# Kernel optimization log

Hardware: AMD Instinct MI355X
Metric: run time of the kernel (lower is better)

Reference implementation:

```python
import jax, jax.numpy as jnp
import numpy as np

N, E, G = 100000, 600000, 2000
CONV = [128, 256, 256, 256]
LIN = [256, 128, 1]
BN_EPS = 1e-5


def setup_inputs() -> dict:
    key = jax.random.key(0)
    ks = iter(jax.random.split(key, 64))
    inp = {}
    inp["x"] = jax.random.normal(next(ks), (N, CONV[0]), dtype=jnp.float32)
    inp["edge_index"] = jax.random.randint(next(ks), (2, E), 0, N)
    inp["batch"] = jnp.sort(jax.random.randint(next(ks), (N,), 0, G))

    def lin_w(k, i, o):
        return (jax.random.normal(k, (i, o), dtype=jnp.float32) / np.sqrt(i)).astype(jnp.float32)

    # 3 GINConv MLPs: Linear(in,out), BN(out), ReLU, Linear(out,out), ReLU
    for i in range(3):
        ci, co = CONV[i], CONV[i + 1]
        inp[f"c{i}_w1"] = lin_w(next(ks), ci, co)
        inp[f"c{i}_b1"] = jnp.zeros((co,), jnp.float32)
        inp[f"c{i}_g"] = jnp.ones((co,), jnp.float32)
        inp[f"c{i}_be"] = jnp.zeros((co,), jnp.float32)
        inp[f"c{i}_m"] = jax.random.normal(next(ks), (co,), dtype=jnp.float32) * 0.1
        inp[f"c{i}_v"] = jax.random.uniform(next(ks), (co,), minval=0.5, maxval=1.5, dtype=jnp.float32)
        inp[f"c{i}_w2"] = lin_w(next(ks), co, co)
        inp[f"c{i}_b2"] = jnp.zeros((co,), jnp.float32)
    # head: Linear(256,128) + BN(128) + ReLU, Linear(128,1)
    inp["l0_w"] = lin_w(next(ks), LIN[0], LIN[1])
    inp["l0_b"] = jnp.zeros((LIN[1],), jnp.float32)
    inp["l0_g"] = jnp.ones((LIN[1],), jnp.float32)
    inp["l0_be"] = jnp.zeros((LIN[1],), jnp.float32)
    inp["l0_m"] = jax.random.normal(next(ks), (LIN[1],), dtype=jnp.float32) * 0.1
    inp["l0_v"] = jax.random.uniform(next(ks), (LIN[1],), minval=0.5, maxval=1.5, dtype=jnp.float32)
    inp["l1_w"] = lin_w(next(ks), LIN[1], LIN[2])
    inp["l1_b"] = jnp.zeros((LIN[2],), jnp.float32)
    return inp


def _bn(h, g, be, m, v):
    return g * (h - m) * jax.lax.rsqrt(v + BN_EPS) + be


def _gin_conv(x, src, dst, w1, b1, g, be, m, v, w2, b2):
    # GINConv (eps=0): MLP(x + sum_{j in N(i)} x_j); messages x[src] aggregated at dst
    agg = jax.ops.segment_sum(x[src], dst, num_segments=x.shape[0])
    h = (x + agg) @ w1 + b1
    h = jax.nn.relu(_bn(h, g, be, m, v))
    return jax.nn.relu(h @ w2 + b2)


def reference(x, edge_index, batch,
              c0_w1, c0_b1, c0_g, c0_be, c0_m, c0_v, c0_w2, c0_b2,
              c1_w1, c1_b1, c1_g, c1_be, c1_m, c1_v, c1_w2, c1_b2,
              c2_w1, c2_b1, c2_g, c2_be, c2_m, c2_v, c2_w2, c2_b2,
              l0_w, l0_b, l0_g, l0_be, l0_m, l0_v, l1_w, l1_b):
    src, dst = edge_index[0], edge_index[1]
    conv_params = [
        (c0_w1, c0_b1, c0_g, c0_be, c0_m, c0_v, c0_w2, c0_b2),
        (c1_w1, c1_b1, c1_g, c1_be, c1_m, c1_v, c1_w2, c1_b2),
        (c2_w1, c2_b1, c2_g, c2_be, c2_m, c2_v, c2_w2, c2_b2),
    ]
    h = x
    for i, p in enumerate(conv_params):
        h = _gin_conv(h, src, dst, *p)
        if i < 2:
            h = jax.nn.relu(h)  # outer activation (no-op after ReLU, kept for fidelity)
    # global_add_pool over graphs
    h = jax.ops.segment_sum(h, batch, num_segments=G)  # [G, 256]
    h = h @ l0_w + l0_b
    h = _bn(h, l0_g, l0_be, l0_m, l0_v)
    h = jax.nn.relu(h)  # dropout is identity in eval mode
    return h @ l1_w + l1_b  # [G, 1]
```

## Files before the change

kernel.cpp:

```cpp
#include <hip/hip_runtime.h>
#include <hip/hip_bf16.h>

#define BN_EPS 1e-5f

typedef __attribute__((ext_vector_type(8))) short short8;
typedef __attribute__((ext_vector_type(4))) float f32x4;

__device__ __forceinline__ void gll16(const void* g, void* l) {
    __builtin_amdgcn_global_load_lds(
        (const __attribute__((address_space(1))) unsigned int*)g,
        (__attribute__((address_space(3))) unsigned int*)l, 16, 0, 0);
}

__device__ __forceinline__ unsigned pack_bf2(float a, float b) {
    __hip_bfloat16 ba = __float2bfloat16(a);
    __hip_bfloat16 bb = __float2bfloat16(b);
    return (unsigned)(*(unsigned short*)&ba) | ((unsigned)(*(unsigned short*)&bb) << 16);
}

__global__ void hist_kernel(const int* __restrict__ dst, int* __restrict__ off, int E) {
    int e = blockIdx.x * blockDim.x + threadIdx.x;
    if (e < E) atomicAdd(&off[dst[e] + 1], 1);
}

__global__ __launch_bounds__(256) void scan1_kernel(int* __restrict__ data,
                                                    int* __restrict__ sums, int n) {
    __shared__ int sh[256];
    const int t = threadIdx.x;
    const int idx = blockIdx.x * 1024 + t * 4;
    int v[4];
    int s = 0;
#pragma unroll
    for (int j = 0; j < 4; ++j) {
        int x = (idx + j < n) ? data[idx + j] : 0;
        s += x;
        v[j] = s;
    }
    sh[t] = s;
    __syncthreads();
    for (int o = 1; o < 256; o <<= 1) {
        int x = (t >= o) ? sh[t - o] : 0;
        __syncthreads();
        sh[t] += x;
        __syncthreads();
    }
    const int prev = sh[t] - s;
#pragma unroll
    for (int j = 0; j < 4; ++j) {
        if (idx + j < n) data[idx + j] = v[j] + prev;
    }
    if (t == 255) sums[blockIdx.x] = sh[255];
}

__global__ __launch_bounds__(256) void scan2_kernel(int* __restrict__ sums, int nb) {
    __shared__ int sh[256];
    const int t = threadIdx.x;
    sh[t] = (t < nb) ? sums[t] : 0;
    __syncthreads();
    for (int o = 1; o < 256; o <<= 1) {
        int x = (t >= o) ? sh[t - o] : 0;
        __syncthreads();
        sh[t] += x;
        __syncthreads();
    }
    if (t < nb) sums[t] = sh[t];
}

__global__ void scan3_kernel(int* __restrict__ data, const int* __restrict__ sums,
                             int* __restrict__ cursor, int n, int N) {
    int i = blockIdx.x * blockDim.x + threadIdx.x;
    if (i >= n) return;
    int b = i >> 10;
    int v = data[i];
    if (b > 0) { v += sums[b - 1]; data[i] = v; }
    if (i < N) cursor[i] = v;
}

__global__ void fill_kernel(const int* __restrict__ src, const int* __restrict__ dst,
                            int* __restrict__ cursor, int* __restrict__ sorted_src, int E) {
    int e = blockIdx.x * blockDim.x + threadIdx.x;
    if (e >= E) return;
    int p = atomicAdd(&cursor[dst[e]], 1);
    sorted_src[p] = src[e];
}

__global__ void cvt_x_kernel(const float* __restrict__ x, __hip_bfloat16* __restrict__ xb,
                             int N, int total4 ) {
    int i = blockIdx.x * blockDim.x + threadIdx.x;
    if (i >= total4) return;
    int n = i >> 5;
    unsigned lo = 0, hi = 0;
    if (n < N) {
        const float4 v = ((const float4*)x)[i];
        lo = pack_bf2(v.x, v.y);
        hi = pack_bf2(v.z, v.w);
    }
    ((uint2*)xb)[i] = make_uint2(lo, hi);
}

__global__ void wt_all_kernel(const float* __restrict__ w0, const float* __restrict__ w1,
                              const float* __restrict__ w2, const float* __restrict__ w3,
                              const float* __restrict__ w4, const float* __restrict__ w5,
                              __hip_bfloat16* __restrict__ o0, __hip_bfloat16* __restrict__ o1,
                              __hip_bfloat16* __restrict__ o2, __hip_bfloat16* __restrict__ o3,
                              __hip_bfloat16* __restrict__ o4, __hip_bfloat16* __restrict__ o5) {
    int i = blockIdx.x * blockDim.x + threadIdx.x;
    const int S0 = 256 * 128, S = 256 * 256;
    if (i < S0) {
        int m = i / 128, k = i - m * 128;
        o0[i] = __float2bfloat16(w0[k * 256 + m]);
        return;
    }
    i -= S0;
    int mi = i / S, j = i - mi * S;
    if (mi >= 5) return;
    int m = j >> 8, k = j & 255;
    const float* Wp; __hip_bfloat16* Op;
    switch (mi) {
        case 0: Wp = w1; Op = o1; break;
        case 1: Wp = w2; Op = o2; break;
        case 2: Wp = w3; Op = o3; break;
        case 3: Wp = w4; Op = o4; break;
        default: Wp = w5; Op = o5; break;
    }
    Op[j] = __float2bfloat16(Wp[k * 256 + m]);
}

__global__ void prep_ss_kernel(
    const float* __restrict__ g0, const float* __restrict__ be0, const float* __restrict__ m0,
    const float* __restrict__ v0, const float* __restrict__ b10, const float* __restrict__ b20,
    const float* __restrict__ g1, const float* __restrict__ be1, const float* __restrict__ m1,
    const float* __restrict__ v1, const float* __restrict__ b11, const float* __restrict__ b21,
    const float* __restrict__ g2, const float* __restrict__ be2, const float* __restrict__ m2,
    const float* __restrict__ v2, const float* __restrict__ b12, const float* __restrict__ b22,
    float* __restrict__ ss) {
    const int layer = blockIdx.x;
    const int c = threadIdx.x;
    const float *g, *be, *m, *v, *b1, *b2;
    switch (layer) {
        case 0: g = g0; be = be0; m = m0; v = v0; b1 = b10; b2 = b20; break;
        case 1: g = g1; be = be1; m = m1; v = v1; b1 = b11; b2 = b21; break;
        default: g = g2; be = be2; m = m2; v = v2; b1 = b12; b2 = b22; break;
    }
    float r = rsqrtf(v[c] + BN_EPS);
    float s = g[c] * r;
    ss[(2 * layer) * 512 + c] = s;
    ss[(2 * layer) * 512 + 256 + c] = (b1[c] - m[c]) * s + be[c];
    ss[(2 * layer + 1) * 512 + c] = 1.f;
    ss[(2 * layer + 1) * 512 + 256 + c] = b2[c];
}

template <int C>
__global__ __launch_bounds__(256) void agg_fused(const __hip_bfloat16* __restrict__ h,
                                                 const int* __restrict__ off,
                                                 const int* __restrict__ ssrc,
                                                 __hip_bfloat16* __restrict__ out, int N) {
    constexpr int L = C / 8;
    int t = blockIdx.x * blockDim.x + threadIdx.x;
    int n = t / L;
    if (n >= N) return;
    int c8 = t - n * L;
    const uint4* hp = (const uint4*)h;

    float acc[8];
    {
        uint4 sv = hp[(size_t)n * L + c8];
        const unsigned u[4] = {sv.x, sv.y, sv.z, sv.w};
#pragma unroll
        for (int j = 0; j < 4; ++j) {
            acc[2 * j]     = __uint_as_float(u[j] << 16);
            acc[2 * j + 1] = __uint_as_float(u[j] & 0xffff0000u);
        }
    }
    const int e0 = off[n], e1 = off[n + 1];
    int e = e0;
    for (; e + 2 <= e1; e += 2) {
        int s0 = ssrc[e], s1 = ssrc[e + 1];
        uint4 a = hp[(size_t)s0 * L + c8];
        uint4 b = hp[(size_t)s1 * L + c8];
        const unsigned ua[4] = {a.x, a.y, a.z, a.w};
        const unsigned ub[4] = {b.x, b.y, b.z, b.w};
#pragma unroll
        for (int j = 0; j < 4; ++j) {
            acc[2 * j]     += __uint_as_float(ua[j] << 16);
            acc[2 * j + 1] += __uint_as_float(ua[j] & 0xffff0000u);
            acc[2 * j]     += __uint_as_float(ub[j] << 16);
            acc[2 * j + 1] += __uint_as_float(ub[j] & 0xffff0000u);
        }
    }
    if (e < e1) {
        int s0 = ssrc[e];
        uint4 a = hp[(size_t)s0 * L + c8];
        const unsigned ua[4] = {a.x, a.y, a.z, a.w};
#pragma unroll
        for (int j = 0; j < 4; ++j) {
            acc[2 * j]     += __uint_as_float(ua[j] << 16);
            acc[2 * j + 1] += __uint_as_float(ua[j] & 0xffff0000u);
        }
    }
    unsigned o[4];
#pragma unroll
    for (int j = 0; j < 4; ++j) o[j] = pack_bf2(acc[2 * j], acc[2 * j + 1]);
    ((uint4*)out)[(size_t)n * L + c8] = make_uint4(o[0], o[1], o[2], o[3]);
}

template <int K1>
__global__ __launch_bounds__(512, 4) void mlp_fused(
    const __hip_bfloat16* __restrict__ A,
    const __hip_bfloat16* __restrict__ W1t,
    const __hip_bfloat16* __restrict__ W2t,
    const float* __restrict__ ss1, const float* __restrict__ ss2,
    __hip_bfloat16* __restrict__ C) {
    __shared__ __align__(16) char bufT[32 * 1024];

    const int tid = threadIdx.x;
    const int l   = tid & 63;
    const int w   = tid >> 6;
    const size_t row0 = (size_t)blockIdx.x * 64;

    constexpr int ROWB = K1 * 2;
    constexpr int NT1  = K1 / 32;
    const int l15  = l & 15;
    const int kg   = l >> 4;
    const int lswz = (l & 7) << 4;

    {
        const char* Ab = (const char*)(A + row0 * K1);
        constexpr int NIA = 64 * ROWB / 1024;
        constexpr int RPI = 1024 / ROWB;
#pragma unroll
        for (int i = w; i < NIA; i += 8) {
            int row = i * RPI + (l * 16) / ROWB;
            int byt = ((l * 16) % ROWB) ^ ((row & 7) << 4);
            gll16(Ab + (size_t)row * ROWB + byt, bufT + i * 1024);
        }
    }
    asm volatile("s_waitcnt vmcnt(0)" ::: "memory");
    __syncthreads();

    f32x4 acc1[2][4] = {};
    {
        const char* wp0 = (const char*)W1t + (size_t)(w * 32 + l15) * ROWB + kg * 16;
        const char* wp1 = wp0 + 16 * ROWB;
#pragma unroll
        for (int t = 0; t < NT1; ++t) {
            const short8 wf0 = *(const short8*)(wp0 + t * 64);
            const short8 wf1 = *(const short8*)(wp1 + t * 64);
            short8 af[4];
            const int abyt = (t * 64 + kg * 16) ^ lswz;
#pragma unroll
            for (int j = 0; j < 4; ++j)
                af[j] = *(const short8*)(bufT + (j * 16 + l15) * ROWB + abyt);
#pragma unroll
            for (int j = 0; j < 4; ++j) {
                acc1[0][j] = __builtin_amdgcn_mfma_f32_16x16x32_bf16(wf0, af[j], acc1[0][j], 0, 0, 0);
                acc1[1][j] = __builtin_amdgcn_mfma_f32_16x16x32_bf16(wf1, af[j], acc1[1][j], 0, 0, 0);
            }
        }
    }
    __syncthreads();

#pragma unroll
    for (int i = 0; i < 2; ++i) {
        const int m0 = w * 32 + i * 16 + kg * 4;
        const float4 s4 = *(const float4*)(ss1 + m0);
        const float4 h4 = *(const float4*)(ss1 + 256 + m0);
        const int byt = (m0 * 2) ^ lswz;
#pragma unroll
        for (int j = 0; j < 4; ++j) {
            const int n = j * 16 + l15;
            const float v0 = fmaxf(acc1[i][j][0] * s4.x + h4.x, 0.f);
            const float v1 = fmaxf(acc1[i][j][1] * s4.y + h4.y, 0.f);
            const float v2 = fmaxf(acc1[i][j][2] * s4.z + h4.z, 0.f);
            const float v3 = fmaxf(acc1[i][j][3] * s4.w + h4.w, 0.f);
            *(uint2*)(bufT + n * 512 + byt) = make_uint2(pack_bf2(v0, v1), pack_bf2(v2, v3));
        }
    }
    __syncthreads();

    f32x4 acc2[2][4] = {};
    {
        const char* wp0 = (const char*)W2t + (size_t)(w * 32 + l15) * 512 + kg * 16;
        const char* wp1 = wp0 + 16 * 512;
#pragma unroll
        for (int t = 0; t < 8; ++t) {
            const short8 wf0 = *(const short8*)(wp0 + t * 64);
            const short8 wf1 = *(const short8*)(wp1 + t * 64);
            short8 tf[4];
            const int tbyt = (t * 64 + kg * 16) ^ lswz;
#pragma unroll
            for (int j = 0; j < 4; ++j)
                tf[j] = *(const short8*)(bufT + (j * 16 + l15) * 512 + tbyt);
#pragma unroll
            for (int j = 0; j < 4; ++j) {
                acc2[0][j] = __builtin_amdgcn_mfma_f32_16x16x32_bf16(wf0, tf[j], acc2[0][j], 0, 0, 0);
                acc2[1][j] = __builtin_amdgcn_mfma_f32_16x16x32_bf16(wf1, tf[j], acc2[1][j], 0, 0, 0);
            }
        }
    }
    __syncthreads();

#pragma unroll
    for (int i = 0; i < 2; ++i) {
        const int c0 = w * 32 + i * 16 + kg * 4;
        const float4 s4 = *(const float4*)(ss2 + c0);
        const float4 h4 = *(const float4*)(ss2 + 256 + c0);
        const int byt = (c0 * 2) ^ lswz;
#pragma unroll
        for (int j = 0; j < 4; ++j) {
            const int n = j * 16 + l15;
            const float v0 = fmaxf(acc2[i][j][0] * s4.x + h4.x, 0.f);
            const float v1 = fmaxf(acc2[i][j][1] * s4.y + h4.y, 0.f);
            const float v2 = fmaxf(acc2[i][j][2] * s4.z + h4.z, 0.f);
            const float v3 = fmaxf(acc2[i][j][3] * s4.w + h4.w, 0.f);
            *(uint2*)(bufT + n * 512 + byt) = make_uint2(pack_bf2(v0, v1), pack_bf2(v2, v3));
        }
    }
    __syncthreads();

    {
        char* Cb = (char*)C + row0 * 512;
#pragma unroll
        for (int q = tid; q < 2048; q += 512) {
            const int n = q >> 5;
            const int slot = (q & 31) * 16;
            uint4 v = *(const uint4*)(bufT + n * 512 + (slot ^ ((n & 7) << 4)));
            *(uint4*)(Cb + q * 16) = v;
        }
    }
}

__device__ __forceinline__ int lower_bound_dev(const int* __restrict__ a, int n, int key) {
    int lo = 0, hi = n;
    while (lo < hi) {
        int mid = (lo + hi) >> 1;
        if (a[mid] < key) lo = mid + 1; else hi = mid;
    }
    return lo;
}

__global__ __launch_bounds__(256) void pool_seg_kernel(const __hip_bfloat16* __restrict__ h,
                                                       const int* __restrict__ batch,
                                                       float* __restrict__ pooled, int N) {
    __shared__ int seg[2];
    const int g = blockIdx.x;
    if (threadIdx.x == 0) seg[0] = lower_bound_dev(batch, N, g);
    if (threadIdx.x == 1) seg[1] = lower_bound_dev(batch, N, g + 1);
    __syncthreads();
    const int c = threadIdx.x;
    float acc = 0.f;
    for (int n = seg[0]; n < seg[1]; ++n) acc += __bfloat162float(h[(size_t)n * 256 + c]);
    pooled[(size_t)g * 256 + c] = acc;
}

__global__ __launch_bounds__(128) void head_kernel(
    const float* __restrict__ pooled,
    const float* __restrict__ w0, const float* __restrict__ b0,
    const float* __restrict__ g, const float* __restrict__ be,
    const float* __restrict__ m, const float* __restrict__ v,
    const float* __restrict__ w1, const float* __restrict__ b1,
    float* __restrict__ out) {
    __shared__ float row[256];
    __shared__ float red[128];
    const int gid = blockIdx.x;
    const int j = threadIdx.x;

    row[j]       = pooled[(size_t)gid * 256 + j];
    row[j + 128] = pooled[(size_t)gid * 256 + 128 + j];
    __syncthreads();

    float acc = b0[j];
#pragma unroll 8
    for (int k = 0; k < 256; ++k) acc += row[k] * w0[k * 128 + j];

    float h = g[j] * (acc - m[j]) * rsqrtf(v[j] + BN_EPS) + be[j];
    h = fmaxf(h, 0.f) * w1[j];
    red[j] = h;
    __syncthreads();
    for (int s = 64; s > 0; s >>= 1) {
        if (j < s) red[j] += red[j + s];
        __syncthreads();
    }
    if (j == 0) out[gid] = red[0] + b1[0];
}

extern "C" void kernel_launch(void* const* d_in, const int* in_sizes, int n_in,
                              void* d_out, int out_size, void* d_ws, size_t ws_size,
                              hipStream_t stream) {
    const float* x    = (const float*)d_in[0];
    const int* eidx   = (const int*)d_in[1];
    const int* batch  = (const int*)d_in[2];

    const int N = in_sizes[0] / 128;
    const int E = in_sizes[1] / 2;
    const int G = out_size;

    const int* src = eidx;
    const int* dst = eidx + E;

    const float* cw1[3]; const float* cb1[3]; const float* cg[3]; const float* cbe[3];
    const float* cm[3];  const float* cv[3];  const float* cw2[3]; const float* cb2[3];
    for (int i = 0; i < 3; ++i) {
        int b = 3 + i * 8;
        cw1[i] = (const float*)d_in[b + 0];
        cb1[i] = (const float*)d_in[b + 1];
        cg[i]  = (const float*)d_in[b + 2];
        cbe[i] = (const float*)d_in[b + 3];
        cm[i]  = (const float*)d_in[b + 4];
        cv[i]  = (const float*)d_in[b + 5];
        cw2[i] = (const float*)d_in[b + 6];
        cb2[i] = (const float*)d_in[b + 7];
    }
    const float* l0_w  = (const float*)d_in[27];
    const float* l0_b  = (const float*)d_in[28];
    const float* l0_g  = (const float*)d_in[29];
    const float* l0_be = (const float*)d_in[30];
    const float* l0_m  = (const float*)d_in[31];
    const float* l0_v  = (const float*)d_in[32];
    const float* l1_w  = (const float*)d_in[33];
    const float* l1_b  = (const float*)d_in[34];

    float* outp = (float*)d_out;

    const int nrb  = (N + 127) / 128;
    const int Npad = nrb * 128;
    const int nrb64 = Npad / 64;
    const size_t SB = (size_t)Npad * 256 * 2;
    const size_t XB = (size_t)Npad * 128 * 2;
    const size_t PB = (size_t)G * 256 * 4;
    const size_t WTB = (size_t)256 * 256 * 2;

    char* ws = (char*)d_ws;
    size_t o = 0;
    __hip_bfloat16* U  = (__hip_bfloat16*)(ws + o); o += SB;
    __hip_bfloat16* V  = (__hip_bfloat16*)(ws + o); o += SB;
    __hip_bfloat16* xb = (__hip_bfloat16*)(ws + o); o += XB;
    float* pooled      = (float*)(ws + o);       o += PB;
    __hip_bfloat16* wt[6];
    for (int i = 0; i < 6; ++i) { wt[i] = (__hip_bfloat16*)(ws + o); o += WTB; }
    float* ss          = (float*)(ws + o);       o += 6 * 512 * 4;
    int* csr_off    = (int*)(ws + o); o += (size_t)(N + 1) * 4;
    int* cursor     = (int*)(ws + o); o += (size_t)N * 4;
    int* sorted_src = (int*)(ws + o); o += (size_t)E * 4;
    int* sums       = (int*)(ws + o); o += 256 * 4;
    if (ws_size < o) return;

    const dim3 blk(256);

    {
        int total4 = Npad * 128 / 4;
        cvt_x_kernel<<<(total4 + 255) / 256, blk, 0, stream>>>(x, xb, N, total4);
    }
    {
        int total = 256 * 128 + 5 * 256 * 256;
        wt_all_kernel<<<(total + 255) / 256, blk, 0, stream>>>(
            cw1[0], cw2[0], cw1[1], cw2[1], cw1[2], cw2[2],
            wt[0], wt[1], wt[2], wt[3], wt[4], wt[5]);
    }
    prep_ss_kernel<<<3, blk, 0, stream>>>(
        cg[0], cbe[0], cm[0], cv[0], cb1[0], cb2[0],
        cg[1], cbe[1], cm[1], cv[1], cb1[1], cb2[1],
        cg[2], cbe[2], cm[2], cv[2], cb1[2], cb2[2], ss);

    {
        const int n_off = N + 1;
        hipMemsetAsync(csr_off, 0, (size_t)n_off * sizeof(int), stream);
        hist_kernel<<<(E + 255) / 256, blk, 0, stream>>>(dst, csr_off, E);
        const int nb = (n_off + 1023) / 1024;
        scan1_kernel<<<nb, blk, 0, stream>>>(csr_off, sums, n_off);
        scan2_kernel<<<1, blk, 0, stream>>>(sums, nb);
        scan3_kernel<<<(n_off + 255) / 256, blk, 0, stream>>>(csr_off, sums, cursor, n_off, N);
        fill_kernel<<<(E + 255) / 256, blk, 0, stream>>>(src, dst, cursor, sorted_src, E);
    }

    auto SS = [&](int i) { return ss + i * 512; };

    {
        int total = N * 16;
        agg_fused<128><<<(total + 255) / 256, blk, 0, stream>>>(xb, csr_off, sorted_src, U, N);
    }
    mlp_fused<128><<<nrb64, dim3(512), 0, stream>>>(U, wt[0], wt[1], SS(0), SS(1), V);

    {
        int total = N * 32;
        agg_fused<256><<<(total + 255) / 256, blk, 0, stream>>>(V, csr_off, sorted_src, U, N);
    }
    mlp_fused<256><<<nrb64, dim3(512), 0, stream>>>(U, wt[2], wt[3], SS(2), SS(3), U);

    {
        int total = N * 32;
        agg_fused<256><<<(total + 255) / 256, blk, 0, stream>>>(U, csr_off, sorted_src, V, N);
    }
    mlp_fused<256><<<nrb64, dim3(512), 0, stream>>>(V, wt[4], wt[5], SS(4), SS(5), V);

    pool_seg_kernel<<<G, blk, 0, stream>>>(V, batch, pooled, N);
    head_kernel<<<G, dim3(128), 0, stream>>>(pooled, l0_w, l0_b, l0_g, l0_be, l0_m, l0_v,
                                             l1_w, l1_b, outp);
}
```

Before: 460.2 us.

## Preload MLP weights into registers and use fragment-ordered LDS layout

Loads each wave's W1/W2 fragments into registers up front, so global weight loads are issued early instead of interleaved with MFMAs. The activation tile in LDS is now stored in MFMA-fragment order (1 KB per 16-row × 32-k block), so each lane reads a contiguous 16-byte slot at l*16 without XOR swizzling. The output store remaps fragment order back to row-major. This raises register pressure (16+16 short8 weight vectors) under launch_bounds(512,4), which risks spills or lower occupancy, and the global output writes become less contiguous.

```diff
diff --git a/kernel.cpp b/kernel.cpp
--- a/kernel.cpp
+++ b/kernel.cpp
@@ -216,86 +216,88 @@
     const int tid = threadIdx.x;
     const int l   = tid & 63;
     const int w   = tid >> 6;
+    const int l15 = l & 15;
+    const int kg  = l >> 4;
     const size_t row0 = (size_t)blockIdx.x * 64;
 
     constexpr int ROWB = K1 * 2;
     constexpr int NT1  = K1 / 32;
-    const int l15  = l & 15;
-    const int kg   = l >> 4;
-    const int lswz = (l & 7) << 4;
+
+    short8 wr1[2][NT1];
+    {
+        const char* Wb = (const char*)W1t + (size_t)(w * 32 + l15) * ROWB + kg * 16;
+#pragma unroll
+        for (int i = 0; i < 2; ++i)
+#pragma unroll
+            for (int t = 0; t < NT1; ++t)
+                wr1[i][t] = *(const short8*)(Wb + (size_t)i * 16 * ROWB + t * 64);
+    }
 
     {
         const char* Ab = (const char*)(A + row0 * K1);
-        constexpr int NIA = 64 * ROWB / 1024;
-        constexpr int RPI = 1024 / ROWB;
-#pragma unroll
-        for (int i = w; i < NIA; i += 8) {
-            int row = i * RPI + (l * 16) / ROWB;
-            int byt = ((l * 16) % ROWB) ^ ((row & 7) << 4);
-            gll16(Ab + (size_t)row * ROWB + byt, bufT + i * 1024);
+#pragma unroll
+        for (int ib = w; ib < 4 * NT1; ib += 8) {
+            const int j = ib / NT1, t = ib % NT1;
+            gll16(Ab + (size_t)(j * 16 + l15) * ROWB + t * 64 + kg * 16,
+                  bufT + ib * 1024);
         }
     }
     asm volatile("s_waitcnt vmcnt(0)" ::: "memory");
     __syncthreads();
 
-    f32x4 acc1[2][4] = {};
-    {
-        const char* wp0 = (const char*)W1t + (size_t)(w * 32 + l15) * ROWB + kg * 16;
-        const char* wp1 = wp0 + 16 * ROWB;
-#pragma unroll
-        for (int t = 0; t < NT1; ++t) {
-            const short8 wf0 = *(const short8*)(wp0 + t * 64);
-            const short8 wf1 = *(const short8*)(wp1 + t * 64);
-            short8 af[4];
-            const int abyt = (t * 64 + kg * 16) ^ lswz;
-#pragma unroll
-            for (int j = 0; j < 4; ++j)
-                af[j] = *(const short8*)(bufT + (j * 16 + l15) * ROWB + abyt);
-#pragma unroll
-            for (int j = 0; j < 4; ++j) {
-                acc1[0][j] = __builtin_amdgcn_mfma_f32_16x16x32_bf16(wf0, af[j], acc1[0][j], 0, 0, 0);
-                acc1[1][j] = __builtin_amdgcn_mfma_f32_16x16x32_bf16(wf1, af[j], acc1[1][j], 0, 0, 0);
-            }
-        }
-    }
-    __syncthreads();
+    f32x4 acc[2][4] = {};
+#pragma unroll
+    for (int t = 0; t < NT1; ++t) {
+        short8 af[4];
+#pragma unroll
+        for (int j = 0; j < 4; ++j)
+            af[j] = *(const short8*)(bufT + (j * NT1 + t) * 1024 + l * 16);
+#pragma unroll
+        for (int j = 0; j < 4; ++j) {
+            acc[0][j] = __builtin_amdgcn_mfma_f32_16x16x32_bf16(wr1[0][t], af[j], acc[0][j], 0, 0, 0);
+            acc[1][j] = __builtin_amdgcn_mfma_f32_16x16x32_bf16(wr1[1][t], af[j], acc[1][j], 0, 0, 0);
+        }
+    }
+    __syncthreads();
+
+    short8 wr2[2][8];
+    {
+        const char* Wb = (const char*)W2t + (size_t)(w * 32 + l15) * 512 + kg * 16;
+#pragma unroll
+        for (int i = 0; i < 2; ++i)
+#pragma unroll
+            for (int t = 0; t < 8; ++t)
+                wr2[i][t] = *(const short8*)(Wb + (size_t)i * 16 * 512 + t * 64);
+    }
 
 #pragma unroll
     for (int i = 0; i < 2; ++i) {
         const int m0 = w * 32 + i * 16 + kg * 4;
         const float4 s4 = *(const float4*)(ss1 + m0);
         const float4 h4 = *(const float4*)(ss1 + 256 + m0);
-        const int byt = (m0 * 2) ^ lswz;
-#pragma unroll
-        for (int j = 0; j < 4; ++j) {
-            const int n = j * 16 + l15;
-            const float v0 = fmaxf(acc1[i][j][0] * s4.x + h4.x, 0.f);
-            const float v1 = fmaxf(acc1[i][j][1] * s4.y + h4.y, 0.f);
-            const float v2 = fmaxf(acc1[i][j][2] * s4.z + h4.z, 0.f);
-            const float v3 = fmaxf(acc1[i][j][3] * s4.w + h4.w, 0.f);
-            *(uint2*)(bufT + n * 512 + byt) = make_uint2(pack_bf2(v0, v1), pack_bf2(v2, v3));
+        const int toff = w * 1024 + (i * 2 + (kg >> 1)) * 256 + l15 * 16 + (kg & 1) * 8;
+#pragma unroll
+        for (int j = 0; j < 4; ++j) {
+            const float v0 = fmaxf(acc[i][j][0] * s4.x + h4.x, 0.f);
+            const float v1 = fmaxf(acc[i][j][1] * s4.y + h4.y, 0.f);
+            const float v2 = fmaxf(acc[i][j][2] * s4.z + h4.z, 0.f);
+            const float v3 = fmaxf(acc[i][j][3] * s4.w + h4.w, 0.f);
+            *(uint2*)(bufT + j * 8192 + toff) = make_uint2(pack_bf2(v0, v1), pack_bf2(v2, v3));
         }
     }
     __syncthreads();
 
     f32x4 acc2[2][4] = {};
-    {
-        const char* wp0 = (const char*)W2t + (size_t)(w * 32 + l15) * 512 + kg * 16;
-        const char* wp1 = wp0 + 16 * 512;
-#pragma unroll
-        for (int t = 0; t < 8; ++t) {
-            const short8 wf0 = *(const short8*)(wp0 + t * 64);
-            const short8 wf1 = *(const short8*)(wp1 + t * 64);
-            short8 tf[4];
-            const int tbyt = (t * 64 + kg * 16) ^ lswz;
-#pragma unroll
-            for (int j = 0; j < 4; ++j)
-                tf[j] = *(const short8*)(bufT + (j * 16 + l15) * 512 + tbyt);
-#pragma unroll
-            for (int j = 0; j < 4; ++j) {
-                acc2[0][j] = __builtin_amdgcn_mfma_f32_16x16x32_bf16(wf0, tf[j], acc2[0][j], 0, 0, 0);
-                acc2[1][j] = __builtin_amdgcn_mfma_f32_16x16x32_bf16(wf1, tf[j], acc2[1][j], 0, 0, 0);
-            }
+#pragma unroll
+    for (int t = 0; t < 8; ++t) {
+        short8 tf[4];
+#pragma unroll
+        for (int j = 0; j < 4; ++j)
+            tf[j] = *(const short8*)(bufT + (j * 8 + t) * 1024 + l * 16);
+#pragma unroll
+        for (int j = 0; j < 4; ++j) {
+            acc2[0][j] = __builtin_amdgcn_mfma_f32_16x16x32_bf16(wr2[0][t], tf[j], acc2[0][j], 0, 0, 0);
+            acc2[1][j] = __builtin_amdgcn_mfma_f32_16x16x32_bf16(wr2[1][t], tf[j], acc2[1][j], 0, 0, 0);
         }
     }
     __syncthreads();
@@ -305,15 +307,14 @@
         const int c0 = w * 32 + i * 16 + kg * 4;
         const float4 s4 = *(const float4*)(ss2 + c0);
         const float4 h4 = *(const float4*)(ss2 + 256 + c0);
-        const int byt = (c0 * 2) ^ lswz;
-#pragma unroll
-        for (int j = 0; j < 4; ++j) {
-            const int n = j * 16 + l15;
+        const int toff = w * 1024 + (i * 2 + (kg >> 1)) * 256 + l15 * 16 + (kg & 1) * 8;
+#pragma unroll
+        for (int j = 0; j < 4; ++j) {
             const float v0 = fmaxf(acc2[i][j][0] * s4.x + h4.x, 0.f);
             const float v1 = fmaxf(acc2[i][j][1] * s4.y + h4.y, 0.f);
             const float v2 = fmaxf(acc2[i][j][2] * s4.z + h4.z, 0.f);
             const float v3 = fmaxf(acc2[i][j][3] * s4.w + h4.w, 0.f);
-            *(uint2*)(bufT + n * 512 + byt) = make_uint2(pack_bf2(v0, v1), pack_bf2(v2, v3));
+            *(uint2*)(bufT + j * 8192 + toff) = make_uint2(pack_bf2(v0, v1), pack_bf2(v2, v3));
         }
     }
     __syncthreads();
@@ -322,10 +323,11 @@
         char* Cb = (char*)C + row0 * 512;
 #pragma unroll
         for (int q = tid; q < 2048; q += 512) {
-            const int n = q >> 5;
-            const int slot = (q & 31) * 16;
-            uint4 v = *(const uint4*)(bufT + n * 512 + (slot ^ ((n & 7) << 4)));
-            *(uint4*)(Cb + q * 16) = v;
+            const int j  = q >> 9;
+            const int wp = (q >> 6) & 7;
+            const int lp = q & 63;
+            uint4 v = *(const uint4*)(bufT + q * 16);
+            *(uint4*)(Cb + (size_t)(j * 16 + (lp & 15)) * 512 + wp * 64 + (lp >> 4) * 16) = v;
         }
     }
 }
```

Result: no change. 464.0 us (+0.8%).
